# Optimization experiments

Hardware: AMD Instinct MI355X
Metric: run time of the kernel (lower is better)

## Reference

```python
import jax, jax.numpy as jnp
import numpy as np

N, K, D = 65536, 1024, 512


def setup_inputs() -> dict:
    key = jax.random.key(0)
    k1, k2, k3 = jax.random.split(key, 3)
    x = jax.random.normal(k1, (N, D), dtype=jnp.float32)
    y = jax.random.randint(k2, (N,), 0, K)  # true/assigned cluster labels
    centers = jax.random.normal(k3, (K, D), dtype=jnp.float32)  # nn.Parameter
    return {"x": x, "y": y, "centers": centers}


def reference(x, y, centers):
    # caldis: squared euclidean distance from every point to every center.
    # original expand+sub+square+sum without materializing [N, K, D]).
    x2 = jnp.sum(x * x, axis=1, keepdims=True)          # [N, 1]
    c2 = jnp.sum(centers * centers, axis=1)              # [K]
    distance = x2 - 2.0 * (x @ centers.T) + c2           # [N, K]

    # predict: torch.sort(distance)[1][:, 0] == index of the smallest distance
    ynew = jnp.argmin(distance, axis=1)                  # [N]

    # calwei + calloss: one-hot(y) * distance summed == gather distance[i, y[i]]
    loss = jnp.sum(jnp.take_along_axis(distance, y[:, None], axis=1))

    return loss, ynew
```

## Files before the change

kernel.cpp:

```cpp
#include <hip/hip_runtime.h>

#define NPTS 65536
#define KC   1024
#define DD   512

using bf16x8 = __attribute__((ext_vector_type(8))) __bf16;
using f32x4  = __attribute__((ext_vector_type(4))) float;

__device__ __forceinline__ void gld_lds16(const void* g, void* lds_base) {
  __builtin_amdgcn_global_load_lds(
      (const __attribute__((address_space(1))) unsigned int*)(uintptr_t)g,
      (__attribute__((address_space(3))) unsigned int*)(unsigned int)(uintptr_t)lds_base,
      16, 0, 0);
}

__device__ __forceinline__ uint2 pack4(const float4& v) {
  uint2 r;
  r.x = (__float_as_uint(v.x) >> 16) | (__float_as_uint(v.y) & 0xffff0000u);
  r.y = (__float_as_uint(v.z) >> 16) | (__float_as_uint(v.w) & 0xffff0000u);
  return r;
}


__global__ __launch_bounds__(256) void prep_kernel(
    const float* __restrict__ x, const int* __restrict__ y,
    const float* __restrict__ centers, uint4* __restrict__ xb,
    uint4* __restrict__ cb, float* __restrict__ c2,
    float* __restrict__ partial) {
  const int w = threadIdx.x >> 6, l = threadIdx.x & 63;
  if (blockIdx.x >= 16384) {
    const int row = (blockIdx.x - 16384) * 4 + w;
    const float4* cf4 = (const float4*)centers;
    float4 a = cf4[row * 128 + 2 * l];
    float4 b = cf4[row * 128 + 2 * l + 1];
    uint2 pa = pack4(a), pb = pack4(b);
    cb[row * 64 + l] = make_uint4(pa.x, pa.y, pb.x, pb.y);
    float s = a.x * a.x + a.y * a.y + a.z * a.z + a.w * a.w +
              b.x * b.x + b.y * b.y + b.z * b.z + b.w * b.w;
#pragma unroll
    for (int off = 32; off; off >>= 1) s += __shfl_down(s, off, 64);
    if (l == 0) c2[row] = s;
    return;
  }
  const int row = blockIdx.x * 4 + w;
  const float4* xr = (const float4*)(x + (size_t)row * DD);
  float4 a = xr[2 * l];
  float4 b = xr[2 * l + 1];
  uint2 pa = pack4(a), pb = pack4(b);
  xb[row * 64 + l] = make_uint4(pa.x, pa.y, pb.x, pb.y);
  const int yr = y[row];
  const float4* cr = (const float4*)(centers + (size_t)yr * DD);
  float4 ca = cr[2 * l];
  float4 cb2 = cr[2 * l + 1];
  float d0 = a.x - ca.x, d1 = a.y - ca.y, d2 = a.z - ca.z, d3 = a.w - ca.w;
  float d4 = b.x - cb2.x, d5 = b.y - cb2.y, d6 = b.z - cb2.z, d7 = b.w - cb2.w;
  float s = d0 * d0 + d1 * d1 + d2 * d2 + d3 * d3 +
            d4 * d4 + d5 * d5 + d6 * d6 + d7 * d7;
#pragma unroll
  for (int off = 32; off; off >>= 1) s += __shfl_down(s, off, 64);
  __shared__ float ps[4];
  if (l == 0) ps[w] = s;
  __syncthreads();
  if (threadIdx.x == 0) partial[blockIdx.x] = ps[0] + ps[1] + ps[2] + ps[3];
}

__global__ __launch_bounds__(256, 2) void gemm_argmin(
    const uint4* __restrict__ xb, const uint4* __restrict__ cb,
    const float* __restrict__ c2, float* __restrict__ ynew_out) {
  __shared__ uint4 As[1024];
  __shared__ uint4 Bs[2048];
  __shared__ float c2s[1024];

  const int t = threadIdx.x;
  const int w = t >> 6, l = t & 63;
  const int wm = w >> 1, wn = w & 1;
  const int q4 = l >> 4, m16 = l & 15;
  const int row0 = blockIdx.x * 128;

#pragma unroll
  for (int i = 0; i < 4; i++) c2s[t + 256 * i] = c2[t + 256 * i];

  const int r_l = l >> 3;
  const int o_l = (l & 7) ^ r_l;
  int aidx[4];
#pragma unroll
  for (int q = 0; q < 4; q++)
    aidx[q] = (row0 + (w * 4 + q) * 8 + r_l) * 64 + o_l;
  int bsrc[8];
#pragma unroll
  for (int q = 0; q < 8; q++)
    bsrc[q] = ((w * 8 + q) * 8 + r_l) * 64 + o_l;

  const int xr = m16 & 7;

  float best[16];
  int bi_[16];
#pragma unroll
  for (int i = 0; i < 16; i++) { best[i] = 3.4e38f; bi_[i] = 0; }

  for (int n0 = 0; n0 < KC; n0 += 256) {
    f32x4 acc[4][8];
#pragma unroll
    for (int i = 0; i < 4; i++)
#pragma unroll
      for (int j = 0; j < 8; j++) acc[i][j] = (f32x4){0.f, 0.f, 0.f, 0.f};

    const uint4* bbase = cb + n0 * 64;

    for (int ks = 0; ks < 8; ks++) {
      __syncthreads();
#pragma unroll
      for (int q = 0; q < 4; q++)
        gld_lds16(xb + aidx[q] + ks * 8, &As[(w * 4 + q) * 64]);
#pragma unroll
      for (int q = 0; q < 8; q++)
        gld_lds16(bbase + bsrc[q] + ks * 8, &Bs[(w * 8 + q) * 64]);
      __syncthreads();
#pragma unroll
      for (int kk = 0; kk < 2; kk++) {
        const int oct = kk * 4 + q4;
        bf16x8 af[4];
#pragma unroll
        for (int i = 0; i < 4; i++) {
          const int ra = wm * 64 + i * 16 + m16;
          af[i] = *(const bf16x8*)&As[ra * 8 + (oct ^ xr)];
        }
#pragma unroll
        for (int j = 0; j < 8; j++) {
          const int rb = wn * 128 + j * 16 + m16;
          bf16x8 bf = *(const bf16x8*)&Bs[rb * 8 + (oct ^ xr)];
#pragma unroll
          for (int i = 0; i < 4; i++)
            acc[i][j] = __builtin_amdgcn_mfma_f32_16x16x32_bf16(af[i], bf, acc[i][j], 0, 0, 0);
        }
      }
    }

#pragma unroll
    for (int j = 0; j < 8; j++) {
      const int n = n0 + wn * 128 + j * 16 + m16;
      const float cc = c2s[n];
#pragma unroll
      for (int i = 0; i < 4; i++)
#pragma unroll
        for (int r = 0; r < 4; r++) {
          float v = fmaf(-2.f, acc[i][j][r], cc);
          const int bi = i * 4 + r;
          if (v < best[bi]) { best[bi] = v; bi_[bi] = n; }
        }
    }
  }

#pragma unroll
  for (int bi = 0; bi < 16; bi++) {
    float v = best[bi];
    int idx = bi_[bi];
#pragma unroll
    for (int off = 8; off; off >>= 1) {
      float ov = __shfl_xor(v, off, 64);
      int oi = __shfl_xor(idx, off, 64);
      if (ov < v || (ov == v && oi < idx)) { v = ov; idx = oi; }
    }
    if (m16 == 0) {
      const int m = wm * 64 + (bi >> 2) * 16 + q4 * 4 + (bi & 3);
      ynew_out[row0 + m] = (float)idx;
    }
  }
}

__global__ __launch_bounds__(256) void loss_final(const float* __restrict__ partial,
                                                  float* __restrict__ out) {
  float s = 0.f;
#pragma unroll
  for (int j = 0; j < 64; j++) s += partial[threadIdx.x + 256 * j];
#pragma unroll
  for (int off = 32; off; off >>= 1) s += __shfl_down(s, off, 64);
  __shared__ float ps[4];
  if ((threadIdx.x & 63) == 0) ps[threadIdx.x >> 6] = s;
  __syncthreads();
  if (threadIdx.x == 0) out[0] = ps[0] + ps[1] + ps[2] + ps[3];
}


#define SLOT(row, oct) (16 * (oct) + (((row) & 15) ^ (((oct) & 2) << 1)))

__device__ __forceinline__ void split_pack(const float4& a, const float4& b,
                                           uint4& hi, uint4& lo) {
  float f[8] = {a.x, a.y, a.z, a.w, b.x, b.y, b.z, b.w};
  uint hw[4], lw[4];
#pragma unroll
  for (int i = 0; i < 4; i++) {
    uint e0 = __float_as_uint(f[2 * i]), e1 = __float_as_uint(f[2 * i + 1]);
    hw[i] = (e0 >> 16) | (e1 & 0xffff0000u);
    float l0 = f[2 * i]     - __uint_as_float(e0 & 0xffff0000u);
    float l1 = f[2 * i + 1] - __uint_as_float(e1 & 0xffff0000u);
    lw[i] = (__float_as_uint(l0) >> 16) | (__float_as_uint(l1) & 0xffff0000u);
  }
  hi = make_uint4(hw[0], hw[1], hw[2], hw[3]);
  lo = make_uint4(lw[0], lw[1], lw[2], lw[3]);
}

__global__ __launch_bounds__(256) void c2_kernel(const float* __restrict__ centers,
                                                 float* __restrict__ c2) {
  int wave = (blockIdx.x * 256 + threadIdx.x) >> 6;
  int lane = threadIdx.x & 63;
  const float4* c4 = (const float4*)(centers + (size_t)wave * DD);
  float s = 0.f;
#pragma unroll
  for (int j = 0; j < 2; j++) {
    float4 v = c4[lane + 64 * j];
    s += v.x * v.x + v.y * v.y + v.z * v.z + v.w * v.w;
  }
#pragma unroll
  for (int off = 32; off; off >>= 1) s += __shfl_down(s, off, 64);
  if (lane == 0) c2[wave] = s;
}

__global__ __launch_bounds__(256, 2) void argmin_fb(
    const float* __restrict__ x, const float* __restrict__ centers,
    const float* __restrict__ c2, float* __restrict__ ynew_out) {
  __shared__ uint4 Ah[512], Al[512], Bh[512], Bl[512];
  const int t = threadIdx.x;
  const int w = t >> 6, l = t & 63;
  const int wm = w >> 1, wn = w & 1;
  const size_t row0 = (size_t)blockIdx.x * 128;
  const int srow = t >> 1, h = t & 1;
  const int mt = srow >> 4;
  const int so0 = mt * 64 + SLOT(srow, 2 * h);
  const int so1 = mt * 64 + SLOT(srow, 2 * h + 1);
  const int rs = SLOT(l & 15, l >> 4);
  const float* xp = x + (row0 + srow) * DD + h * 16;
  float best[16];
  int bidx[16];
#pragma unroll
  for (int i = 0; i < 16; i++) { best[i] = 3.4e38f; bidx[i] = 0; }
  for (int n0 = 0; n0 < KC; n0 += 128) {
    const float* bp = centers + (size_t)(n0 + srow) * DD + h * 16;
    f32x4 acc[4][4];
#pragma unroll
    for (int i = 0; i < 4; i++)
#pragma unroll
      for (int j = 0; j < 4; j++) acc[i][j] = (f32x4){0.f, 0.f, 0.f, 0.f};
    float4 ra[4], rb[4];
#pragma unroll
    for (int q = 0; q < 4; q++) {
      ra[q] = *(const float4*)(xp + q * 4);
      rb[q] = *(const float4*)(bp + q * 4);
    }
    for (int ks = 0; ks < 16; ks++) {
      uint4 ah0, al0, ah1, al1, bh0, bl0, bh1, bl1;
      split_pack(ra[0], ra[1], ah0, al0);
      split_pack(ra[2], ra[3], ah1, al1);
      split_pack(rb[0], rb[1], bh0, bl0);
      split_pack(rb[2], rb[3], bh1, bl1);
      __syncthreads();
      Ah[so0] = ah0; Al[so0] = al0;
      Ah[so1] = ah1; Al[so1] = al1;
      Bh[so0] = bh0; Bl[so0] = bl0;
      Bh[so1] = bh1; Bl[so1] = bl1;
      __syncthreads();
      if (ks < 15) {
#pragma unroll
        for (int q = 0; q < 4; q++) {
          ra[q] = *(const float4*)(xp + (ks + 1) * 32 + q * 4);
          rb[q] = *(const float4*)(bp + (ks + 1) * 32 + q * 4);
        }
      }
      bf16x8 afh[4], afl[4], bfh[4], bfl[4];
#pragma unroll
      for (int i = 0; i < 4; i++) {
        afh[i] = *(const bf16x8*)&Ah[(wm * 4 + i) * 64 + rs];
        afl[i] = *(const bf16x8*)&Al[(wm * 4 + i) * 64 + rs];
        bfh[i] = *(const bf16x8*)&Bh[(wn * 4 + i) * 64 + rs];
        bfl[i] = *(const bf16x8*)&Bl[(wn * 4 + i) * 64 + rs];
      }
#pragma unroll
      for (int i = 0; i < 4; i++)
#pragma unroll
        for (int j = 0; j < 4; j++) {
          acc[i][j] = __builtin_amdgcn_mfma_f32_16x16x32_bf16(afh[i], bfh[j], acc[i][j], 0, 0, 0);
          acc[i][j] = __builtin_amdgcn_mfma_f32_16x16x32_bf16(afl[i], bfh[j], acc[i][j], 0, 0, 0);
          acc[i][j] = __builtin_amdgcn_mfma_f32_16x16x32_bf16(afh[i], bfl[j], acc[i][j], 0, 0, 0);
        }
    }
#pragma unroll
    for (int j = 0; j < 4; j++) {
      int n = n0 + wn * 64 + j * 16 + (l & 15);
      float cc = c2[n];
#pragma unroll
      for (int i = 0; i < 4; i++)
#pragma unroll
        for (int r = 0; r < 4; r++) {
          float v = fmaf(-2.f, acc[i][j][r], cc);
          int bi = i * 4 + r;
          if (v < best[bi]) { best[bi] = v; bidx[bi] = n; }
        }
    }
  }
#pragma unroll
  for (int bi = 0; bi < 16; bi++) {
    float v = best[bi];
    int idx = bidx[bi];
#pragma unroll
    for (int off = 8; off; off >>= 1) {
      float ov = __shfl_xor(v, off, 64);
      int oi = __shfl_xor(idx, off, 64);
      if (ov < v || (ov == v && oi < idx)) { v = ov; idx = oi; }
    }
    if ((l & 15) == 0) {
      int m = wm * 64 + (bi >> 2) * 16 + (l >> 4) * 4 + (bi & 3);
      ynew_out[row0 + m] = (float)idx;
    }
  }
}

__global__ __launch_bounds__(256) void loss_partial_fb(
    const float* __restrict__ x, const int* __restrict__ y,
    const float* __restrict__ centers, float* __restrict__ partial) {
  const int w = threadIdx.x >> 6, l = threadIdx.x & 63;
  const int row = blockIdx.x * 4 + w;
  const float4* x4 = (const float4*)(x + (size_t)row * DD);
  const float4* c4 = (const float4*)(centers + (size_t)y[row] * DD);
  float s = 0.f;
#pragma unroll
  for (int j = 0; j < 2; j++) {
    float4 xv = x4[2 * l + j], cv = c4[2 * l + j];
    float dx = xv.x - cv.x, dy = xv.y - cv.y, dz = xv.z - cv.z, dw = xv.w - cv.w;
    s += dx * dx + dy * dy + dz * dz + dw * dw;
  }
#pragma unroll
  for (int off = 32; off; off >>= 1) s += __shfl_down(s, off, 64);
  __shared__ float ps[4];
  if (l == 0) ps[w] = s;
  __syncthreads();
  if (threadIdx.x == 0) partial[blockIdx.x] = ps[0] + ps[1] + ps[2] + ps[3];
}


extern "C" void kernel_launch(void* const* d_in, const int* in_sizes, int n_in,
                              void* d_out, int out_size, void* d_ws, size_t ws_size,
                              hipStream_t stream) {
  const float* x       = (const float*)d_in[0];
  const int*   y       = (const int*)d_in[1];
  const float* centers = (const float*)d_in[2];
  float* out = (float*)d_out;

  const size_t xb_bytes = (size_t)NPTS * DD * 2;
  const size_t cb_bytes = (size_t)KC * DD * 2;
  const size_t need = xb_bytes + cb_bytes + (KC + NPTS / 4) * sizeof(float);

  if (ws_size >= need) {
    uint4* xb      = (uint4*)d_ws;
    uint4* cbp     = (uint4*)((char*)d_ws + xb_bytes);
    float* c2      = (float*)((char*)d_ws + xb_bytes + cb_bytes);
    float* partial = c2 + KC;
    prep_kernel<<<16384 + 256, 256, 0, stream>>>(x, y, centers, xb, cbp, c2, partial);
    gemm_argmin<<<NPTS / 128, 256, 0, stream>>>(xb, cbp, c2, out + 1);
    loss_final<<<1, 256, 0, stream>>>(partial, out);
  } else {
    float* c2      = (float*)d_ws;
    float* partial = c2 + KC;
    c2_kernel<<<KC / 4, 256, 0, stream>>>(centers, c2);
    argmin_fb<<<NPTS / 128, 256, 0, stream>>>(x, centers, c2, out + 1);
    loss_partial_fb<<<NPTS / 4, 256, 0, stream>>>(x, y, centers, partial);
    loss_final<<<1, 256, 0, stream>>>(partial, out);
  }
}
```

Before: 275.1 us.

## Pipeline GEMM-argmin with 4-stage async LDS ring and 512-thread 256-row tiles

Rewrites the fused GEMM+argmin kernel to use 512 threads over 256-row tiles, with a 4-slot LDS ring buffer. Global-to-LDS loads for step tt+2 are issued while MFMAs run on the current step, using vmcnt waits and a single barrier per step instead of two syncthreads. It also adds setprio around the MFMA blocks and a cross-wave argmin merge through LDS, because two column-halves now cover the whole K range per row. The aim is to hide load latency and cut barrier overhead. The cost is more LDS per block and hand-tuned wait counts, which are fragile.

```diff
diff --git a/kernel.cpp b/kernel.cpp
--- a/kernel.cpp
+++ b/kernel.cpp
@@ -64,93 +64,113 @@
   if (threadIdx.x == 0) partial[blockIdx.x] = ps[0] + ps[1] + ps[2] + ps[3];
 }
 
-__global__ __launch_bounds__(256, 2) void gemm_argmin(
+__global__ __launch_bounds__(512, 2) void gemm_argmin(
     const uint4* __restrict__ xb, const uint4* __restrict__ cb,
     const float* __restrict__ c2, float* __restrict__ ynew_out) {
-  __shared__ uint4 As[1024];
-  __shared__ uint4 Bs[2048];
-  __shared__ float c2s[1024];
+  __shared__ uint4 As[4096];
+  __shared__ uint4 Bs[4096];
+  __shared__ float c2s[KC];
 
   const int t = threadIdx.x;
   const int w = t >> 6, l = t & 63;
   const int wm = w >> 1, wn = w & 1;
   const int q4 = l >> 4, m16 = l & 15;
-  const int row0 = blockIdx.x * 128;
-
-#pragma unroll
-  for (int i = 0; i < 4; i++) c2s[t + 256 * i] = c2[t + 256 * i];
-
-  const int r_l = l >> 3;
-  const int o_l = (l & 7) ^ r_l;
-  int aidx[4];
-#pragma unroll
-  for (int q = 0; q < 4; q++)
-    aidx[q] = (row0 + (w * 4 + q) * 8 + r_l) * 64 + o_l;
-  int bsrc[8];
-#pragma unroll
-  for (int q = 0; q < 8; q++)
-    bsrc[q] = ((w * 8 + q) * 8 + r_l) * 64 + o_l;
-
-  const int xr = m16 & 7;
+  const int row0 = blockIdx.x * 256;
+
+  c2s[t] = c2[t];
+  c2s[t + 512] = c2[t + 512];
+
+  const uint4* aB = xb + ((size_t)(row0 + w * 16 + (l >> 2)) * 64 + (l & 3));
+  const uint4* bB = cb + ((size_t)(w * 16 + (l >> 2)) * 64 + (l & 3));
+
+  gld_lds16(aB, &As[w * 64]);
+  gld_lds16(aB + 8192, &As[w * 64 + 512]);
+  gld_lds16(bB, &Bs[w * 64]);
+  gld_lds16(bB + 8192, &Bs[w * 64 + 512]);
+  gld_lds16(aB + 4, &As[1024 + w * 64]);
+  gld_lds16(aB + 8196, &As[1024 + w * 64 + 512]);
+  gld_lds16(bB + 4, &Bs[1024 + w * 64]);
+  gld_lds16(bB + 8196, &Bs[1024 + w * 64 + 512]);
+
+  f32x4 acc[4][8];
+#pragma unroll
+  for (int i = 0; i < 4; i++)
+#pragma unroll
+    for (int j = 0; j < 8; j++) acc[i][j] = (f32x4){0.f, 0.f, 0.f, 0.f};
 
   float best[16];
   int bi_[16];
 #pragma unroll
   for (int i = 0; i < 16; i++) { best[i] = 3.4e38f; bi_[i] = 0; }
 
-  for (int n0 = 0; n0 < KC; n0 += 256) {
-    f32x4 acc[4][8];
+  asm volatile("s_waitcnt vmcnt(4)" ::: "memory");
+  __builtin_amdgcn_s_barrier();
+
+#pragma unroll 4
+  for (int tt = 0; tt < 64; ++tt) {
+    const int bse = (tt & 3) * 1024;
+    bf16x8 af[4], bf0[4], bf1[4];
 #pragma unroll
     for (int i = 0; i < 4; i++)
-#pragma unroll
-      for (int j = 0; j < 8; j++) acc[i][j] = (f32x4){0.f, 0.f, 0.f, 0.f};
-
-    const uint4* bbase = cb + n0 * 64;
-
-    for (int ks = 0; ks < 8; ks++) {
-      __syncthreads();
-#pragma unroll
-      for (int q = 0; q < 4; q++)
-        gld_lds16(xb + aidx[q] + ks * 8, &As[(w * 4 + q) * 64]);
-#pragma unroll
-      for (int q = 0; q < 8; q++)
-        gld_lds16(bbase + bsrc[q] + ks * 8, &Bs[(w * 8 + q) * 64]);
-      __syncthreads();
-#pragma unroll
-      for (int kk = 0; kk < 2; kk++) {
-        const int oct = kk * 4 + q4;
-        bf16x8 af[4];
-#pragma unroll
-        for (int i = 0; i < 4; i++) {
-          const int ra = wm * 64 + i * 16 + m16;
-          af[i] = *(const bf16x8*)&As[ra * 8 + (oct ^ xr)];
-        }
-#pragma unroll
-        for (int j = 0; j < 8; j++) {
-          const int rb = wn * 128 + j * 16 + m16;
-          bf16x8 bf = *(const bf16x8*)&Bs[rb * 8 + (oct ^ xr)];
-#pragma unroll
-          for (int i = 0; i < 4; i++)
-            acc[i][j] = __builtin_amdgcn_mfma_f32_16x16x32_bf16(af[i], bf, acc[i][j], 0, 0, 0);
-        }
+      af[i] = *(const bf16x8*)&As[bse + (wm * 64 + i * 16 + m16) * 4 + q4];
+#pragma unroll
+    for (int j = 0; j < 4; j++)
+      bf0[j] = *(const bf16x8*)&Bs[bse + (wn * 128 + j * 16 + m16) * 4 + q4];
+    if (tt < 62) {
+      const int s2 = ((tt + 2) & 3) * 1024;
+      const int oa = ((tt + 2) & 15) * 4;
+      gld_lds16(aB + oa, &As[s2 + w * 64]);
+      gld_lds16(aB + 8192 + oa, &As[s2 + w * 64 + 512]);
+    }
+    __builtin_amdgcn_s_setprio(1);
+#pragma unroll
+    for (int j = 0; j < 4; j++)
+#pragma unroll
+      for (int i = 0; i < 4; i++)
+        acc[i][j] = __builtin_amdgcn_mfma_f32_16x16x32_bf16(af[i], bf0[j], acc[i][j], 0, 0, 0);
+    __builtin_amdgcn_s_setprio(0);
+#pragma unroll
+    for (int j = 0; j < 4; j++)
+      bf1[j] = *(const bf16x8*)&Bs[bse + (wn * 128 + (j + 4) * 16 + m16) * 4 + q4];
+    if (tt < 62) {
+      const int s2 = ((tt + 2) & 3) * 1024;
+      const int ob = ((tt + 2) >> 4) * 16384 + ((tt + 2) & 15) * 4;
+      gld_lds16(bB + ob, &Bs[s2 + w * 64]);
+      gld_lds16(bB + ob + 8192, &Bs[s2 + w * 64 + 512]);
+    }
+    __builtin_amdgcn_s_setprio(1);
+#pragma unroll
+    for (int j = 0; j < 4; j++)
+#pragma unroll
+      for (int i = 0; i < 4; i++)
+        acc[i][j + 4] = __builtin_amdgcn_mfma_f32_16x16x32_bf16(af[i], bf1[j], acc[i][j + 4], 0, 0, 0);
+    __builtin_amdgcn_s_setprio(0);
+
+    if ((tt & 15) == 15) {
+      const int n0 = (tt >> 4) * 256;
+#pragma unroll
+      for (int j = 0; j < 8; j++) {
+        const int n = n0 + wn * 128 + j * 16 + m16;
+        const float cc = c2s[n];
+#pragma unroll
+        for (int i = 0; i < 4; i++)
+#pragma unroll
+          for (int r = 0; r < 4; r++) {
+            float v = fmaf(-2.f, acc[i][j][r], cc);
+            const int bi = i * 4 + r;
+            if (v < best[bi]) { best[bi] = v; bi_[bi] = n; }
+            acc[i][j][r] = 0.f;
+          }
       }
     }
 
-#pragma unroll
-    for (int j = 0; j < 8; j++) {
-      const int n = n0 + wn * 128 + j * 16 + m16;
-      const float cc = c2s[n];
-#pragma unroll
-      for (int i = 0; i < 4; i++)
-#pragma unroll
-        for (int r = 0; r < 4; r++) {
-          float v = fmaf(-2.f, acc[i][j][r], cc);
-          const int bi = i * 4 + r;
-          if (v < best[bi]) { best[bi] = v; bi_[bi] = n; }
-        }
-    }
-  }
-
+    if (tt < 62) asm volatile("s_waitcnt vmcnt(4)" ::: "memory");
+    else         asm volatile("s_waitcnt vmcnt(0)" ::: "memory");
+    __builtin_amdgcn_s_barrier();
+  }
+
+  float* mv = (float*)As;
+  int*   mi = (int*)((char*)As + 2048);
 #pragma unroll
   for (int bi = 0; bi < 16; bi++) {
     float v = best[bi];
@@ -163,8 +183,16 @@
     }
     if (m16 == 0) {
       const int m = wm * 64 + (bi >> 2) * 16 + q4 * 4 + (bi & 3);
-      ynew_out[row0 + m] = (float)idx;
-    }
+      mv[wn * 256 + m] = v;
+      mi[wn * 256 + m] = idx;
+    }
+  }
+  __syncthreads();
+  if (t < 256) {
+    float v0 = mv[t], v1 = mv[256 + t];
+    int i0 = mi[t], i1 = mi[256 + t];
+    const int idx = (v1 < v0 || (v1 == v0 && i1 < i0)) ? i1 : i0;
+    ynew_out[row0 + t] = (float)idx;
   }
 }
 
@@ -355,7 +383,7 @@
     float* c2      = (float*)((char*)d_ws + xb_bytes + cb_bytes);
     float* partial = c2 + KC;
     prep_kernel<<<16384 + 256, 256, 0, stream>>>(x, y, centers, xb, cbp, c2, partial);
-    gemm_argmin<<<NPTS / 128, 256, 0, stream>>>(xb, cbp, c2, out + 1);
+    gemm_argmin<<<NPTS / 256, 512, 0, stream>>>(xb, cbp, c2, out + 1);
     loss_final<<<1, 256, 0, stream>>>(partial, out);
   } else {
     float* c2      = (float*)d_ws;
```

After: 270.7 us. Within noise of the previous version (-1.6%).
